# Performance work log

Measured on AMD Instinct MI355X. Metric: run time of the kernel, lower is better.

Reference implementation:

```python
import jax, jax.numpy as jnp
import numpy as np

B, Q, C, H, D, E, I = 8, 256, 192, 20, 64, 1500, 5120
HID = H * D  # 1280
EPS = 1e-5
SCALE = D ** -0.5


def _linear(x, w, b):
    return jnp.einsum('bsh,oh->bso', x, w) + b


def _layernorm(x, w, b):
    xf = x.astype(jnp.float32)
    mu = jnp.mean(xf, axis=-1, keepdims=True)
    var = jnp.mean(jnp.square(xf - mu), axis=-1, keepdims=True)
    return ((xf - mu) * jax.lax.rsqrt(var + EPS) * w + b).astype(x.dtype)


def _heads(x):  # [B,S,HID] -> [B,H,S,D]
    return x.reshape(B, -1, H, D).transpose(0, 2, 1, 3)


def setup_inputs() -> dict:
    key = jax.random.key(0)
    ks = jax.random.split(key, 24)
    s = 0.02
    inp = {
        'hidden_states': jax.random.normal(ks[0], (B, Q, HID), jnp.float32),
        'mask': jnp.zeros((B, 1, Q, Q + C), jnp.float32),
        'past_key': jax.random.normal(ks[1], (B, H, C, D), jnp.float32),
        'past_value': jax.random.normal(ks[2], (B, H, C, D), jnp.float32),
        'cross_key': jax.random.normal(ks[3], (B, H, E, D), jnp.float32),
        'cross_value': jax.random.normal(ks[4], (B, H, E, D), jnp.float32),
        'q_w': jax.random.normal(ks[5], (HID, HID), jnp.float32) * s,
        'q_b': jnp.zeros((HID,), jnp.float32),
        'k_w': jax.random.normal(ks[6], (HID, HID), jnp.float32) * s,
        'k_b': jnp.zeros((HID,), jnp.float32),
        'v_w': jax.random.normal(ks[7], (HID, HID), jnp.float32) * s,
        'v_b': jnp.zeros((HID,), jnp.float32),
        'o_w': jax.random.normal(ks[8], (HID, HID), jnp.float32) * s,
        'o_b': jnp.zeros((HID,), jnp.float32),
        'cq_w': jax.random.normal(ks[9], (HID, HID), jnp.float32) * s,
        'cq_b': jnp.zeros((HID,), jnp.float32),
        'co_w': jax.random.normal(ks[10], (HID, HID), jnp.float32) * s,
        'co_b': jnp.zeros((HID,), jnp.float32),
        'up_w': jax.random.normal(ks[11], (I, HID), jnp.float32) * s,
        'up_b': jnp.zeros((I,), jnp.float32),
        'down_w': jax.random.normal(ks[12], (HID, I), jnp.float32) * s,
        'down_b': jnp.zeros((HID,), jnp.float32),
        'ln1_w': jnp.ones((HID,), jnp.float32),
        'ln1_b': jnp.zeros((HID,), jnp.float32),
        'ln2_w': jnp.ones((HID,), jnp.float32),
        'ln2_b': jnp.zeros((HID,), jnp.float32),
        'ln3_w': jnp.ones((HID,), jnp.float32),
        'ln3_b': jnp.zeros((HID,), jnp.float32),
    }
    return inp


def reference(hidden_states, mask, past_key, past_value, cross_key, cross_value,
              q_w, q_b, k_w, k_b, v_w, v_b, o_w, o_b,
              cq_w, cq_b, co_w, co_b, up_w, up_b, down_w, down_b,
              ln1_w, ln1_b, ln2_w, ln2_b, ln3_w, ln3_b):
    # ---- self-attention block ----
    residual = hidden_states
    x = _layernorm(hidden_states, ln1_w, ln1_b)
    q = _heads(_linear(x, q_w, q_b) * SCALE)          # [B,H,Q,D]
    k_new = _heads(_linear(x, k_w, k_b))              # [B,H,Q,D]
    v_new = _heads(_linear(x, v_w, v_b))
    k = jnp.concatenate([past_key, k_new], axis=2)    # [B,H,C+Q,D]
    v = jnp.concatenate([past_value, v_new], axis=2)
    scores = jnp.einsum('bhqd,bhkd->bhqk', q, k) + mask
    attn = jnp.einsum('bhqk,bhkd->bhqd', jax.nn.softmax(scores, axis=-1), v)
    attn = attn.transpose(0, 2, 1, 3).reshape(B, Q, HID)
    attn_out = _linear(attn, o_w, o_b)
    present_key = k[:, :, Q:, :]
    present_value = v[:, :, Q:, :]
    h = residual + attn_out
    # ---- cross-attention block ----
    residual = h
    x = _layernorm(h, ln2_w, ln2_b)
    cq = _heads(_linear(x, cq_w, cq_b) * SCALE)       # [B,H,Q,D]
    cscores = jnp.einsum('bhqd,bhkd->bhqk', cq, cross_key)
    cattn = jnp.einsum('bhqk,bhkd->bhqd', jax.nn.softmax(cscores, axis=-1), cross_value)
    cattn = cattn.transpose(0, 2, 1, 3).reshape(B, Q, HID)
    h = residual + _linear(cattn, co_w, co_b)
    # ---- MLP block ----
    residual = h
    x = _layernorm(h, ln3_w, ln3_b)
    up = _linear(x, up_w, up_b)
    mlp_out = _linear(jax.nn.gelu(up, approximate=False), down_w, down_b)
    h = residual + mlp_out
    return (h, present_key, present_value)
```

## Files before the change

### kernel.cpp

```cpp
#include <hip/hip_runtime.h>
#include <math.h>

#define Bc   8
#define Qn   256
#define Cn   192
#define Hn   20
#define Dn   64
#define En   1500
#define In   5120
#define HIDn 1280
#define BQ   2048
#define KSELF 448
#define S1   (BQ*HIDn)
#define WSZ  (HIDn*HIDn)

typedef __attribute__((ext_vector_type(8))) short bf16x8;
typedef __attribute__((ext_vector_type(4))) float f32x4;

__device__ __forceinline__ short f2bf(float f) {
  union { float f; unsigned u; } x; x.f = f;
  unsigned r = x.u + 0x7fffu + ((x.u >> 16) & 1u);
  return (short)(r >> 16);
}
__device__ __forceinline__ float bf2f(short s) {
  union { unsigned u; float f; } x; x.u = ((unsigned)(unsigned short)s) << 16;
  return x.f;
}
__device__ __forceinline__ void gload16(const short* g, short* l) {
  __builtin_amdgcn_global_load_lds(
      (const __attribute__((address_space(1))) void*)g,
      (__attribute__((address_space(3))) void*)l, 16, 0, 0);
}

__global__ __launch_bounds__(256) void convert_all(
    const float* q, const float* k, const float* v, const float* o,
    const float* cq, const float* co, const float* up, const float* dn,
    short* wq, short* wk, short* wv, short* wo,
    short* wcq, short* wco, short* wup, short* wdn)
{
  const float* src; short* dst; int n;
  switch (blockIdx.y) {
    case 0: src = q;  dst = wq;  n = WSZ; break;
    case 1: src = k;  dst = wk;  n = WSZ; break;
    case 2: src = v;  dst = wv;  n = WSZ; break;
    case 3: src = o;  dst = wo;  n = WSZ; break;
    case 4: src = cq; dst = wcq; n = WSZ; break;
    case 5: src = co; dst = wco; n = WSZ; break;
    case 6: src = up; dst = wup; n = HIDn * In; break;
    default: src = dn; dst = wdn; n = HIDn * In; break;
  }
  const int i = (blockIdx.x * 256 + threadIdx.x) * 8;
  if (i >= n) return;
  const float4 a = *reinterpret_cast<const float4*>(src + i);
  const float4 b = *reinterpret_cast<const float4*>(src + i + 4);
  bf16x8 t;
  t[0] = f2bf(a.x); t[1] = f2bf(a.y); t[2] = f2bf(a.z); t[3] = f2bf(a.w);
  t[4] = f2bf(b.x); t[5] = f2bf(b.y); t[6] = f2bf(b.z); t[7] = f2bf(b.w);
  *reinterpret_cast<bf16x8*>(dst + i) = t;
}

__global__ __launch_bounds__(256) void layernorm_k(
    const float* __restrict__ in, const float* __restrict__ w,
    const float* __restrict__ b, short* __restrict__ out)
{
  const int row = blockIdx.x;
  const float* x = in + (size_t)row * HIDn;
  float v[5], s = 0.f, s2 = 0.f;
#pragma unroll
  for (int i = 0; i < 5; ++i) {
    float t = x[threadIdx.x + 256 * i];
    v[i] = t; s += t; s2 += t * t;
  }
#pragma unroll
  for (int off = 1; off < 64; off <<= 1) {
    s  += __shfl_xor(s,  off, 64);
    s2 += __shfl_xor(s2, off, 64);
  }
  __shared__ float red[8];
  const int wave = threadIdx.x >> 6, lane = threadIdx.x & 63;
  if (lane == 0) { red[wave] = s; red[wave + 4] = s2; }
  __syncthreads();
  s  = red[0] + red[1] + red[2] + red[3];
  s2 = red[4] + red[5] + red[6] + red[7];
  const float mu  = s / HIDn;
  const float var = s2 / HIDn - mu * mu;
  const float rs  = rsqrtf(var + 1e-5f);
#pragma unroll
  for (int i = 0; i < 5; ++i) {
    const int c = threadIdx.x + 256 * i;
    out[(size_t)row * HIDn + c] = f2bf((v[i] - mu) * rs * w[c] + b[c]);
  }
}

template<int BM, int BN, int MODE>
__global__ __launch_bounds__(256) void gemm_lds(
    const short* __restrict__ A, const short* __restrict__ W,
    const float* __restrict__ bias, const float* __restrict__ resid,
    void* __restrict__ out0, void* __restrict__ out1, void* __restrict__ out2,
    const float* __restrict__ b1, const float* __restrict__ b2,
    int N, int K, float scale)
{
  constexpr int FM = BM / 32, FN = BN / 32;
  constexpr int NIA = BM / 16, NIB = BN / 16;
  __shared__ __align__(16) short Alds[BM * 32];
  __shared__ __align__(16) short Blds[BN * 32];
  const int tid = threadIdx.x, lane = tid & 63, wave = tid >> 6;
  const int wr = wave >> 1, wc = wave & 1;
  const int m0 = blockIdx.x * BM, n0 = blockIdx.y * BN;
  const int lr = lane & 15;
  const int kc = (lane >> 4) * 8;

  f32x4 acc[FM][FN];
#pragma unroll
  for (int mi = 0; mi < FM; ++mi)
#pragma unroll
    for (int ni = 0; ni < FN; ++ni)
      acc[mi][ni] = (f32x4){0.f, 0.f, 0.f, 0.f};

  const int nk = K >> 5;
  for (int kt = 0; kt < nk; ++kt) {
    const int k0 = kt << 5;
#pragma unroll
    for (int j = 0; j < NIA / 4; ++j) {
      const int ia  = wave + 4 * j;
      const int row = (ia / FM) * (BM / 2) + (ia % FM) * 16 + lr;
      gload16(A + (size_t)(m0 + row) * K + k0 + kc, &Alds[ia * 512]);
    }
#pragma unroll
    for (int j = 0; j < NIB / 4; ++j) {
      const int ib  = wave + 4 * j;
      const int row = (ib / FN) * (BN / 2) + (ib % FN) * 16 + lr;
      gload16(W + (size_t)(n0 + row) * K + k0 + kc, &Blds[ib * 512]);
    }
    __syncthreads();
    bf16x8 af[FM], bfv[FN];
#pragma unroll
    for (int mi = 0; mi < FM; ++mi)
      af[mi] = *reinterpret_cast<const bf16x8*>(&Alds[((wr * FM + mi) * 64 + lane) * 8]);
#pragma unroll
    for (int ni = 0; ni < FN; ++ni)
      bfv[ni] = *reinterpret_cast<const bf16x8*>(&Blds[((wc * FN + ni) * 64 + lane) * 8]);
#pragma unroll
    for (int mi = 0; mi < FM; ++mi)
#pragma unroll
      for (int ni = 0; ni < FN; ++ni)
        acc[mi][ni] = __builtin_amdgcn_mfma_f32_16x16x32_bf16(af[mi], bfv[ni], acc[mi][ni], 0, 0, 0);
    __syncthreads();
  }

  const int cn = lane & 15;
  const int rb = (lane >> 4) * 4;
#pragma unroll
  for (int mi = 0; mi < FM; ++mi)
#pragma unroll
    for (int ni = 0; ni < FN; ++ni)
#pragma unroll
      for (int j = 0; j < 4; ++j) {
        const int row = m0 + wr * (BM / 2) + mi * 16 + rb + j;
        const int col = n0 + wc * (BN / 2) + ni * 16 + cn;
        const float a = acc[mi][ni][j];
        if (MODE == 0) {
          ((float*)out0)[(size_t)row * N + col] =
              a + bias[col] + resid[(size_t)row * N + col];
        } else if (MODE == 1) {
          ((short*)out0)[(size_t)row * N + col] = f2bf((a + bias[col]) * scale);
        } else if (MODE == 2) {
          float t = a + bias[col];
          t = 0.5f * t * (1.f + erff(t * 0.70710678118654752f));
          ((short*)out0)[(size_t)row * N + col] = f2bf(t);
        } else {
          const int rg  = n0 / 1280;
          const int cl  = col - rg * 1280;
          short* op     = rg == 0 ? (short*)out0 : rg == 1 ? (short*)out1 : (short*)out2;
          const float* bp = rg == 0 ? bias : rg == 1 ? b1 : b2;
          const float sc  = rg == 0 ? 0.125f : 1.f;
          op[(size_t)row * 1280 + cl] = f2bf((a + bp[cl]) * sc);
        }
      }
}

template<bool HASMASK>
__global__ __launch_bounds__(256) void attn_mfma(
    const short* __restrict__ Qb, const float* __restrict__ Kp,
    const float* __restrict__ Vp, const short* __restrict__ Kn,
    const short* __restrict__ Vn, const float* __restrict__ mask,
    short* __restrict__ Ob, int Cp, int KT)
{
  const int qt = blockIdx.x, h = blockIdx.y, b = blockIdx.z;
  const int tid = threadIdx.x, lane = tid & 63, wave = tid >> 6;
  const int q0 = qt * 64;
  const int cn = lane & 15;
  const int hg = lane >> 4;
  const int rb = hg * 4;

  __shared__ __align__(16) short k_s[64][72];
  __shared__ __align__(16) short vt_s[64][72];
  __shared__ __align__(16) short p_s[4][16][72];

  bf16x8 aq[2];
  {
    const short* qrow = Qb + (size_t)(b * Qn + q0 + wave * 16 + cn) * HIDn + h * 64;
    aq[0] = *reinterpret_cast<const bf16x8*>(qrow + hg * 8);
    aq[1] = *reinterpret_cast<const bf16x8*>(qrow + 32 + hg * 8);
  }

  float mrun[4] = {-1e30f, -1e30f, -1e30f, -1e30f};
  float lrun[4] = {0.f, 0.f, 0.f, 0.f};
  f32x4 oacc[4];
#pragma unroll
  for (int t = 0; t < 4; ++t) oacc[t] = (f32x4){0.f, 0.f, 0.f, 0.f};

  const int nchunk = (KT + 63) >> 6;
  for (int ci = 0; ci < nchunk; ++ci) {
    const int c0 = ci * 64;
    for (int i = tid; i < 64 * 8; i += 256) {
      const int key = i >> 3, d8 = (i & 7) * 8;
      const int gk = c0 + key;
      bf16x8 kv8 = (bf16x8)0, vv8 = (bf16x8)0;
      if (gk < KT) {
        if (gk < Cp) {
          const size_t off = (((size_t)b * Hn + h) * (size_t)Cp + gk) * 64 + d8;
          const float4 ka = *reinterpret_cast<const float4*>(Kp + off);
          const float4 kb = *reinterpret_cast<const float4*>(Kp + off + 4);
          const float4 va = *reinterpret_cast<const float4*>(Vp + off);
          const float4 vb = *reinterpret_cast<const float4*>(Vp + off + 4);
          kv8[0] = f2bf(ka.x); kv8[1] = f2bf(ka.y); kv8[2] = f2bf(ka.z); kv8[3] = f2bf(ka.w);
          kv8[4] = f2bf(kb.x); kv8[5] = f2bf(kb.y); kv8[6] = f2bf(kb.z); kv8[7] = f2bf(kb.w);
          vv8[0] = f2bf(va.x); vv8[1] = f2bf(va.y); vv8[2] = f2bf(va.z); vv8[3] = f2bf(va.w);
          vv8[4] = f2bf(vb.x); vv8[5] = f2bf(vb.y); vv8[6] = f2bf(vb.z); vv8[7] = f2bf(vb.w);
        } else {
          const size_t off = (size_t)(b * Qn + (gk - Cp)) * HIDn + h * 64 + d8;
          kv8 = *reinterpret_cast<const bf16x8*>(Kn + off);
          vv8 = *reinterpret_cast<const bf16x8*>(Vn + off);
        }
      }
      *reinterpret_cast<bf16x8*>(&k_s[key][d8]) = kv8;
      const int g = key >> 3, o = key & 7, f = (d8 >> 3) & 7;
#pragma unroll
      for (int j = 0; j < 8; ++j)
        vt_s[d8 + j][((g ^ f) << 3) | o] = vv8[j];
    }
    __syncthreads();

    f32x4 sacc[4];
#pragma unroll
    for (int t = 0; t < 4; ++t) sacc[t] = (f32x4){0.f, 0.f, 0.f, 0.f};
#pragma unroll
    for (int t = 0; t < 4; ++t)
#pragma unroll
      for (int kk = 0; kk < 2; ++kk) {
        const bf16x8 bk = *reinterpret_cast<const bf16x8*>(&k_s[t * 16 + cn][kk * 32 + hg * 8]);
        sacc[t] = __builtin_amdgcn_mfma_f32_16x16x32_bf16(aq[kk], bk, sacc[t], 0, 0, 0);
      }

    float sc[4][4];
#pragma unroll
    for (int t = 0; t < 4; ++t) {
      const int key = c0 + t * 16 + cn;
      const bool valid = key < KT;
#pragma unroll
      for (int j = 0; j < 4; ++j) {
        float v = sacc[t][j];
        if (HASMASK && valid)
          v += mask[((size_t)(b * Qn) + q0 + wave * 16 + rb + j) * KT + key];
        sc[t][j] = valid ? v : -1e30f;
      }
    }

#pragma unroll
    for (int j = 0; j < 4; ++j) {
      float mx = fmaxf(fmaxf(sc[0][j], sc[1][j]), fmaxf(sc[2][j], sc[3][j]));
#pragma unroll
      for (int off = 1; off < 16; off <<= 1) mx = fmaxf(mx, __shfl_xor(mx, off, 64));
      const float mnew  = fmaxf(mrun[j], mx);
      const float alpha = __expf(mrun[j] - mnew);
      float ps = 0.f;
#pragma unroll
      for (int t = 0; t < 4; ++t) {
        const float p = __expf(sc[t][j] - mnew);
        sc[t][j] = p; ps += p;
      }
#pragma unroll
      for (int off = 1; off < 16; off <<= 1) ps += __shfl_xor(ps, off, 64);
      lrun[j] = lrun[j] * alpha + ps;
      mrun[j] = mnew;
#pragma unroll
      for (int t = 0; t < 4; ++t) oacc[t][j] *= alpha;
    }

#pragma unroll
    for (int t = 0; t < 4; ++t)
#pragma unroll
      for (int j = 0; j < 4; ++j)
        p_s[wave][rb + j][t * 16 + cn] = f2bf(sc[t][j]);

    const bf16x8 ap0 = *reinterpret_cast<const bf16x8*>(&p_s[wave][cn][hg * 8]);
    const bf16x8 ap1 = *reinterpret_cast<const bf16x8*>(&p_s[wave][cn][32 + hg * 8]);
#pragma unroll
    for (int t = 0; t < 4; ++t) {
      const int d  = t * 16 + cn;
      const int fd = (d >> 3) & 7;
      const bf16x8 bv0 = *reinterpret_cast<const bf16x8*>(&vt_s[d][((hg)     ^ fd) << 3]);
      const bf16x8 bv1 = *reinterpret_cast<const bf16x8*>(&vt_s[d][((4 + hg) ^ fd) << 3]);
      oacc[t] = __builtin_amdgcn_mfma_f32_16x16x32_bf16(ap0, bv0, oacc[t], 0, 0, 0);
      oacc[t] = __builtin_amdgcn_mfma_f32_16x16x32_bf16(ap1, bv1, oacc[t], 0, 0, 0);
    }
    __syncthreads();
  }

#pragma unroll
  for (int t = 0; t < 4; ++t)
#pragma unroll
    for (int j = 0; j < 4; ++j)
      Ob[(size_t)(b * Qn + q0 + wave * 16 + rb + j) * HIDn + h * 64 + t * 16 + cn] =
          f2bf(oacc[t][j] / lrun[j]);
}

__global__ __launch_bounds__(256) void copy_present(
    const short* __restrict__ kn, const short* __restrict__ vn,
    float* __restrict__ outk, float* __restrict__ outv)
{
  const int idx = blockIdx.x * 256 + threadIdx.x;
  if (idx >= Bc * Hn * Cn * 8) return;
  const int d8 = (idx & 7) * 8;
  int t = idx >> 3;
  const int c = t % Cn; t /= Cn;
  const int h = t % Hn;
  const int b = t / Hn;
  const size_t src = (size_t)(b * Qn + (Qn - Cn) + c) * HIDn + h * 64 + d8;
  const size_t dst = (((size_t)b * Hn + h) * Cn + c) * 64 + d8;
  const bf16x8 kv = *reinterpret_cast<const bf16x8*>(kn + src);
  const bf16x8 vv = *reinterpret_cast<const bf16x8*>(vn + src);
#pragma unroll
  for (int j = 0; j < 8; ++j) {
    outk[dst + j] = bf2f(kv[j]);
    outv[dst + j] = bf2f(vv[j]);
  }
}

extern "C" void kernel_launch(void* const* d_in, const int* in_sizes, int n_in,
                              void* d_out, int out_size, void* d_ws, size_t ws_size,
                              hipStream_t stream)
{
  const float* hidden  = (const float*)d_in[0];
  const float* mask    = (const float*)d_in[1];
  const float* past_k  = (const float*)d_in[2];
  const float* past_v  = (const float*)d_in[3];
  const float* cross_k = (const float*)d_in[4];
  const float* cross_v = (const float*)d_in[5];
  const float* q_w  = (const float*)d_in[6];  const float* q_b  = (const float*)d_in[7];
  const float* k_w  = (const float*)d_in[8];  const float* k_b  = (const float*)d_in[9];
  const float* v_w  = (const float*)d_in[10]; const float* v_b  = (const float*)d_in[11];
  const float* o_w  = (const float*)d_in[12]; const float* o_b  = (const float*)d_in[13];
  const float* cq_w = (const float*)d_in[14]; const float* cq_b = (const float*)d_in[15];
  const float* co_w = (const float*)d_in[16]; const float* co_b = (const float*)d_in[17];
  const float* up_w = (const float*)d_in[18]; const float* up_b = (const float*)d_in[19];
  const float* dn_w = (const float*)d_in[20]; const float* dn_b = (const float*)d_in[21];
  const float* ln1w = (const float*)d_in[22]; const float* ln1b = (const float*)d_in[23];
  const float* ln2w = (const float*)d_in[24]; const float* ln2b = (const float*)d_in[25];
  const float* ln3w = (const float*)d_in[26]; const float* ln3b = (const float*)d_in[27];

  short* wq  = (short*)d_ws;
  short* wk  = wq  + (size_t)WSZ;
  short* wv  = wk  + (size_t)WSZ;
  short* wo  = wv  + (size_t)WSZ;
  short* wcq = wo  + (size_t)WSZ;
  short* wco = wcq + (size_t)WSZ;
  short* wup = wco + (size_t)WSZ;
  short* wdn = wup + (size_t)HIDn * In;
  short* xb  = wdn + (size_t)HIDn * In;
  short* qb  = xb  + (size_t)S1;
  short* kb  = qb  + (size_t)S1;
  short* vb  = kb  + (size_t)S1;
  short* ab  = vb  + (size_t)S1;
  short* upa = ab  + (size_t)S1;
  float* h1  = (float*)(upa + (size_t)BQ * In);
  float* h2  = h1 + (size_t)S1;

  float* out_h  = (float*)d_out;
  float* out_pk = out_h + (size_t)S1;
  float* out_pv = out_pk + (size_t)(Bc * Hn * Cn * Dn);

  const dim3 blk(256);
  const dim3 gconv(3200, 8);
  const dim3 gqkv(16, 30);
  const dim3 g64(32, 20);
  const dim3 gup(16, 40);
  const dim3 gattn(Qn / 64, Hn, Bc);

  convert_all<<<gconv, blk, 0, stream>>>(q_w, k_w, v_w, o_w, cq_w, co_w, up_w, dn_w,
                                         wq, wk, wv, wo, wcq, wco, wup, wdn);
  layernorm_k<<<BQ, blk, 0, stream>>>(hidden, ln1w, ln1b, xb);
  gemm_lds<128, 128, 3><<<gqkv, blk, 0, stream>>>(xb, wq, q_b, nullptr,
      qb, kb, vb, k_b, v_b, 3840, HIDn, 1.f);
  copy_present<<<(Bc * Hn * Cn * 8 + 255) / 256, blk, 0, stream>>>(kb, vb, out_pk, out_pv);
  attn_mfma<true><<<gattn, blk, 0, stream>>>(qb, past_k, past_v, kb, vb, mask, ab, Cn, KSELF);
  gemm_lds<64, 64, 0><<<g64, blk, 0, stream>>>(ab, wo, o_b, hidden,
      h1, nullptr, nullptr, nullptr, nullptr, HIDn, HIDn, 1.f);
  layernorm_k<<<BQ, blk, 0, stream>>>(h1, ln2w, ln2b, xb);
  gemm_lds<64, 64, 1><<<g64, blk, 0, stream>>>(xb, wcq, cq_b, nullptr,
      qb, nullptr, nullptr, nullptr, nullptr, HIDn, HIDn, 0.125f);
  attn_mfma<false><<<gattn, blk, 0, stream>>>(qb, cross_k, cross_v,
      (const short*)nullptr, (const short*)nullptr, nullptr, ab, En, En);
  gemm_lds<64, 64, 0><<<g64, blk, 0, stream>>>(ab, wco, co_b, h1,
      h2, nullptr, nullptr, nullptr, nullptr, HIDn, HIDn, 1.f);
  layernorm_k<<<BQ, blk, 0, stream>>>(h2, ln3w, ln3b, xb);
  gemm_lds<128, 128, 2><<<gup, blk, 0, stream>>>(xb, wup, up_b, nullptr,
      upa, nullptr, nullptr, nullptr, nullptr, In, HIDn, 1.f);
  gemm_lds<64, 64, 0><<<g64, blk, 0, stream>>>(upa, wdn, dn_b, h2,
      out_h, nullptr, nullptr, nullptr, nullptr, HIDn, In, 1.f);
}
```

Measured before the change: 525.3 us.

## Deepen GEMM K-tile to 64, enlarge N-side tiles, swizzle attention block order

The GEMM kernel now stages a 64-deep K slice per iteration instead of 32, which halves the number of barrier pairs and issues two MFMA k-steps per LDS fill. The LDS layout is reorganized to match. The 1280-wide GEMMs move from 64x64 to 128x64 tiles for more reuse per block, which also halves their grid size. The attention grid is flattened to 1D with an index swizzle so that consecutive blocks spread across head/batch groups, likely for XCD or cache locality. The cost is doubled LDS per block, which may lower occupancy, and fewer blocks for the N=1280 GEMMs.

```diff
diff --git a/kernel.cpp b/kernel.cpp
--- a/kernel.cpp
+++ b/kernel.cpp
@@ -93,7 +93,7 @@
 }
 
 template<int BM, int BN, int MODE>
-__global__ __launch_bounds__(256) void gemm_lds(
+__global__ __launch_bounds__(256) void gemm_bk64(
     const short* __restrict__ A, const short* __restrict__ W,
     const float* __restrict__ bias, const float* __restrict__ resid,
     void* __restrict__ out0, void* __restrict__ out1, void* __restrict__ out2,
@@ -101,9 +101,8 @@
     int N, int K, float scale)
 {
   constexpr int FM = BM / 32, FN = BN / 32;
-  constexpr int NIA = BM / 16, NIB = BN / 16;
-  __shared__ __align__(16) short Alds[BM * 32];
-  __shared__ __align__(16) short Blds[BN * 32];
+  __shared__ __align__(16) short Alds[BM * 64];
+  __shared__ __align__(16) short Blds[BN * 64];
   const int tid = threadIdx.x, lane = tid & 63, wave = tid >> 6;
   const int wr = wave >> 1, wc = wave & 1;
   const int m0 = blockIdx.x * BM, n0 = blockIdx.y * BN;
@@ -117,34 +116,42 @@
     for (int ni = 0; ni < FN; ++ni)
       acc[mi][ni] = (f32x4){0.f, 0.f, 0.f, 0.f};
 
-  const int nk = K >> 5;
+  const int nk = K >> 6;
   for (int kt = 0; kt < nk; ++kt) {
-    const int k0 = kt << 5;
-#pragma unroll
-    for (int j = 0; j < NIA / 4; ++j) {
-      const int ia  = wave + 4 * j;
-      const int row = (ia / FM) * (BM / 2) + (ia % FM) * 16 + lr;
-      gload16(A + (size_t)(m0 + row) * K + k0 + kc, &Alds[ia * 512]);
-    }
-#pragma unroll
-    for (int j = 0; j < NIB / 4; ++j) {
-      const int ib  = wave + 4 * j;
-      const int row = (ib / FN) * (BN / 2) + (ib % FN) * 16 + lr;
-      gload16(W + (size_t)(n0 + row) * K + k0 + kc, &Blds[ib * 512]);
+    const int k0 = kt << 6;
+#pragma unroll
+    for (int j = 0; j < BM / 32; ++j) {
+      const int i = wave + 4 * j;
+      const int rb = i >> 1, kk = i & 1;
+      gload16(A + (size_t)(m0 + rb * 16 + lr) * K + k0 + kk * 32 + kc, &Alds[i * 512]);
+    }
+#pragma unroll
+    for (int j = 0; j < BN / 32; ++j) {
+      const int i = wave + 4 * j;
+      const int rb = i >> 1, kk = i & 1;
+      gload16(W + (size_t)(n0 + rb * 16 + lr) * K + k0 + kk * 32 + kc, &Blds[i * 512]);
     }
     __syncthreads();
-    bf16x8 af[FM], bfv[FN];
-#pragma unroll
-    for (int mi = 0; mi < FM; ++mi)
-      af[mi] = *reinterpret_cast<const bf16x8*>(&Alds[((wr * FM + mi) * 64 + lane) * 8]);
-#pragma unroll
-    for (int ni = 0; ni < FN; ++ni)
-      bfv[ni] = *reinterpret_cast<const bf16x8*>(&Blds[((wc * FN + ni) * 64 + lane) * 8]);
-#pragma unroll
-    for (int mi = 0; mi < FM; ++mi)
+    bf16x8 af[2][FM], bfv[2][FN];
+#pragma unroll
+    for (int kk = 0; kk < 2; ++kk) {
+#pragma unroll
+      for (int mi = 0; mi < FM; ++mi)
+        af[kk][mi] = *reinterpret_cast<const bf16x8*>(
+            &Alds[((wr * FM + mi) * 2 + kk) * 512 + lane * 8]);
 #pragma unroll
       for (int ni = 0; ni < FN; ++ni)
-        acc[mi][ni] = __builtin_amdgcn_mfma_f32_16x16x32_bf16(af[mi], bfv[ni], acc[mi][ni], 0, 0, 0);
+        bfv[kk][ni] = *reinterpret_cast<const bf16x8*>(
+            &Blds[((wc * FN + ni) * 2 + kk) * 512 + lane * 8]);
+    }
+#pragma unroll
+    for (int kk = 0; kk < 2; ++kk)
+#pragma unroll
+      for (int mi = 0; mi < FM; ++mi)
+#pragma unroll
+        for (int ni = 0; ni < FN; ++ni)
+          acc[mi][ni] = __builtin_amdgcn_mfma_f32_16x16x32_bf16(
+              af[kk][mi], bfv[kk][ni], acc[mi][ni], 0, 0, 0);
     __syncthreads();
   }
 
@@ -186,7 +193,11 @@
     const short* __restrict__ Vn, const float* __restrict__ mask,
     short* __restrict__ Ob, int Cp, int KT)
 {
-  const int qt = blockIdx.x, h = blockIdx.y, b = blockIdx.z;
+  const int orig = blockIdx.x;
+  const int idx  = (orig & 7) * 80 + (orig >> 3);
+  const int qt = idx & 3;
+  const int h  = (idx >> 2) % Hn;
+  const int b  = idx / (4 * Hn);
   const int tid = threadIdx.x, lane = tid & 63, wave = tid >> 6;
   const int q0 = qt * 64;
   const int cn = lane & 15;
@@ -384,29 +395,29 @@
   const dim3 blk(256);
   const dim3 gconv(3200, 8);
   const dim3 gqkv(16, 30);
-  const dim3 g64(32, 20);
+  const dim3 gn64(16, 20);
   const dim3 gup(16, 40);
-  const dim3 gattn(Qn / 64, Hn, Bc);
+  const dim3 gattn(640);
 
   convert_all<<<gconv, blk, 0, stream>>>(q_w, k_w, v_w, o_w, cq_w, co_w, up_w, dn_w,
                                          wq, wk, wv, wo, wcq, wco, wup, wdn);
   layernorm_k<<<BQ, blk, 0, stream>>>(hidden, ln1w, ln1b, xb);
-  gemm_lds<128, 128, 3><<<gqkv, blk, 0, stream>>>(xb, wq, q_b, nullptr,
+  gemm_bk64<128, 128, 3><<<gqkv, blk, 0, stream>>>(xb, wq, q_b, nullptr,
       qb, kb, vb, k_b, v_b, 3840, HIDn, 1.f);
   copy_present<<<(Bc * Hn * Cn * 8 + 255) / 256, blk, 0, stream>>>(kb, vb, out_pk, out_pv);
   attn_mfma<true><<<gattn, blk, 0, stream>>>(qb, past_k, past_v, kb, vb, mask, ab, Cn, KSELF);
-  gemm_lds<64, 64, 0><<<g64, blk, 0, stream>>>(ab, wo, o_b, hidden,
+  gemm_bk64<128, 64, 0><<<gn64, blk, 0, stream>>>(ab, wo, o_b, hidden,
       h1, nullptr, nullptr, nullptr, nullptr, HIDn, HIDn, 1.f);
   layernorm_k<<<BQ, blk, 0, stream>>>(h1, ln2w, ln2b, xb);
-  gemm_lds<64, 64, 1><<<g64, blk, 0, stream>>>(xb, wcq, cq_b, nullptr,
+  gemm_bk64<128, 64, 1><<<gn64, blk, 0, stream>>>(xb, wcq, cq_b, nullptr,
       qb, nullptr, nullptr, nullptr, nullptr, HIDn, HIDn, 0.125f);
   attn_mfma<false><<<gattn, blk, 0, stream>>>(qb, cross_k, cross_v,
       (const short*)nullptr, (const short*)nullptr, nullptr, ab, En, En);
-  gemm_lds<64, 64, 0><<<g64, blk, 0, stream>>>(ab, wco, co_b, h1,
+  gemm_bk64<128, 64, 0><<<gn64, blk, 0, stream>>>(ab, wco, co_b, h1,
       h2, nullptr, nullptr, nullptr, nullptr, HIDn, HIDn, 1.f);
   layernorm_k<<<BQ, blk, 0, stream>>>(h2, ln3w, ln3b, xb);
-  gemm_lds<128, 128, 2><<<gup, blk, 0, stream>>>(xb, wup, up_b, nullptr,
+  gemm_bk64<128, 128, 2><<<gup, blk, 0, stream>>>(xb, wup, up_b, nullptr,
       upa, nullptr, nullptr, nullptr, nullptr, In, HIDn, 1.f);
-  gemm_lds<64, 64, 0><<<g64, blk, 0, stream>>>(upa, wdn, dn_b, h2,
+  gemm_bk64<128, 64, 0><<<gn64, blk, 0, stream>>>(upa, wdn, dn_b, h2,
       out_h, nullptr, nullptr, nullptr, nullptr, HIDn, In, 1.f);
 }
```

New measurement: 521.5 us. Within noise of the previous version (-0.7%).
